# Kernel tuning notes

Measured on AMD Instinct MI355X. Metric: run time of the kernel, lower is better.

Reference implementation:

```python
import jax, jax.numpy as jnp
import numpy as np

B, T, V = 64, 8192, 50257


def setup_inputs() -> dict:
    key = jax.random.key(0)
    k1, k2, k3, k4 = jax.random.split(key, 4)
    ids = jax.random.randint(k1, (B, T), 1, V, dtype=jnp.int32)
    # give each row a random real length in [T//2, T], rest padding (pad_token_id=0)
    lens = jax.random.randint(k4, (B,), T // 2, T + 1, dtype=jnp.int32)
    pos = jnp.arange(T, dtype=jnp.int32)[None, :]
    input_ids = jnp.where(pos < lens[:, None], ids, 0)
    is_punct = jax.random.uniform(k2, (V,)) < 0.05
    is_abbreviation = jax.random.uniform(k3, (V,)) < 0.01
    return {
        "input_ids": input_ids,
        "is_punct": is_punct,
        "is_abbreviation": is_abbreviation,
        "max_phrase_len": 32,
        "pad_token_id": 0,
    }


def reference(input_ids, is_punct, is_abbreviation, max_phrase_len, pad_token_id):
    Bb, Tt = input_ids.shape
    # ---- compute_is_end ----
    punct_at_t = is_punct[input_ids]                               # (B,T)
    prev_ids = jnp.concatenate(
        [jnp.zeros((Bb, 1), input_ids.dtype), input_ids[:, :-1]], axis=1)
    prev_is_abbr = is_abbreviation[prev_ids].at[:, 0].set(False)
    is_real = input_ids != pad_token_id                            # (B,T)
    pos = jnp.arange(Tt, dtype=jnp.int32)
    pos_bt = jnp.broadcast_to(pos[None, :], (Bb, Tt))
    last_real = jnp.max(jnp.where(is_real, pos_bt, -1), axis=1)    # (B,)
    is_end0 = punct_at_t & ~prev_is_abbr & is_real                 # pre-scan boundaries

    def step(last_boundary, xs):
        e_t, t = xs
        forced = (t - last_boundary) >= max_phrase_len
        fire = (e_t | (last_real == t) | forced) & (t <= last_real)
        last_boundary = jnp.where(fire, t, last_boundary)
        return last_boundary, fire

    _, fires = jax.lax.scan(
        step, jnp.full((Bb,), -1, jnp.int32),
        (is_end0.T, jnp.arange(Tt, dtype=jnp.int32)))
    is_end = fires.T                                               # (B,T) bool

    # ---- pack_phrases_from_is_end (P padded to T upper bound) ----
    ie = is_end.astype(jnp.int32)
    phrase_id = jnp.concatenate(
        [jnp.zeros((Bb, 1), jnp.int32), jnp.cumsum(ie[:, :-1], axis=1)], axis=1)
    P = Tt
    rows = jnp.arange(Bb, dtype=jnp.int32)[:, None]
    first_pos = jnp.full((Bb, P), Tt, jnp.int32).at[rows, phrase_id].min(pos_bt)
    slot = pos_bt - jnp.take_along_axis(first_pos, phrase_id, axis=1)  # (B,T)
    in_range = (slot < max_phrase_len) & (slot >= 0) & is_real
    # route invalid entries to a dummy slot (index max_phrase_len), slice it off
    safe_slot = jnp.where(in_range, slot, max_phrase_len)
    mask_pad = jnp.zeros((Bb, P, max_phrase_len + 1), bool)
    mask_pad = mask_pad.at[rows, phrase_id, safe_slot].set(in_range)
    phrase_mask = mask_pad[:, :, :max_phrase_len]
    tok_pad = jnp.zeros((Bb, P, max_phrase_len + 1), jnp.int32)
    tok_pad = tok_pad.at[rows, phrase_id, safe_slot].set(jnp.where(in_range, pos_bt, 0))
    phrase_token_idx = tok_pad[:, :, :max_phrase_len]
    phrase_end_pos = jnp.full((Bb, P), -1, jnp.int32).at[rows, phrase_id].max(
        jnp.where(in_range, pos_bt, -1))
    return phrase_mask, phrase_token_idx, phrase_end_pos
```

## Files before the change

kernel.cpp:

```cpp
#include <hip/hip_runtime.h>
#include <stdint.h>

#define BB 64
#define TT 8192

#define WS_PAIR   4096

#define MOFF ((long long)BB * TT * 32)

__device__ __forceinline__ unsigned long long bitsBelow(int e) {
    return (e >= 64) ? ~0ULL : ((1ULL << e) - 1ULL);
}

__device__ __forceinline__ bool lut(const void* tbl, int flag, int idx) {
    if (flag == 2) return ((const float*)tbl)[idx]   != 0.0f;
    if (flag == 1) return ((const uint8_t*)tbl)[idx] != 0;
    return ((const int*)tbl)[idx] != 0;
}

__global__ __launch_bounds__(256) void bg_kernel(
        const int* __restrict__ ids,
        const void* __restrict__ punct,
        const void* __restrict__ abbr,
        ulonglong2* __restrict__ pairW,
        int* __restrict__ out) {
    __shared__ int sFlag;
    if (threadIdx.x == 0) sFlag = 0;
    __syncthreads();
    {
        const uint32_t* w = (const uint32_t*)punct;
        bool byteGT1 = false, wordGT1 = false;
#pragma unroll
        for (int j = 0; j < 4; ++j) {
            uint32_t x = w[threadIdx.x * 4 + j];
            byteGT1 |= (x & 0xFEFEFEFEu) != 0u;
            wordGT1 |= (x > 1u);
        }
        int local = (byteGT1 ? 2 : 0) | (wordGT1 ? 1 : 0);
        if (local) atomicOr(&sFlag, local);
    }
    __syncthreads();
    int fl = sFlag;
    int flag = (fl & 2) ? 2 : (fl & 1);

    {
        long long zbase = (long long)blockIdx.x * 16384;
        int4 z = make_int4(0, 0, 0, 0);
#pragma unroll
        for (int k = 0; k < 16; ++k) {
            *(int4*)(out + zbase + k * 1024 + threadIdx.x * 4) = z;
        }
        out[2 * MOFF + blockIdx.x * 256 + threadIdx.x] = -1;
    }

    int g = blockIdx.x * 256 + threadIdx.x;
    int t = g & (TT - 1);
    int id = ids[g];
    bool real = (id != 0);
    bool isLR = real && ((t == TT - 1) || (ids[g + 1] == 0));
    bool e = false;
    if (real) {
        bool pu = lut(punct, flag, id);
        if (pu) {
            bool pa = (t > 0) ? lut(abbr, flag, ids[g - 1]) : false;
            e = !pa;
        }
    }
    bool natural = real && (e || isLR);
    unsigned long long nb = __ballot(natural);
    unsigned long long rb = __ballot(real);
    if ((threadIdx.x & 63) == 0) {
        pairW[g >> 6] = make_ulonglong2(nb, rb);
    }
}

__global__ __launch_bounds__(1024) void sparse_kernel(
        const ulonglong2* __restrict__ pairW,
        int* __restrict__ out) {
    __shared__ int sFires[TT];
    __shared__ int sNf;

    int b    = blockIdx.x;
    int tid  = threadIdx.x;
    int wave = tid >> 6, lane = tid & 63;

    if (wave == 0) {
        ulonglong2 pA = pairW[b * 128 + lane];
        ulonglong2 pB = pairW[b * 128 + 64 + lane];
        unsigned long long nA = pA.x, rA = pA.y;
        unsigned long long nB = pB.x, rB = pB.y;
        int lnA = nA ? lane * 64 + 63 - __clzll(nA) : -1;
        int lnB = nB ? (lane + 64) * 64 + 63 - __clzll(nB) : -1;
        int sA = lnA;
        for (int d = 1; d < 64; d <<= 1) { int v = __shfl_up(sA, d); if (lane >= d) sA = max(sA, v); }
        int exA = __shfl_up(sA, 1); if (lane == 0) exA = -1;
        int totA = __shfl(sA, 63);
        int sB = lnB;
        for (int d = 1; d < 64; d <<= 1) { int v = __shfl_up(sB, d); if (lane >= d) sB = max(sB, v); }
        int exB = __shfl_up(sB, 1); if (lane == 0) exB = -1;
        exB = max(exB, totA);

        auto fireWord = [&](unsigned long long nw, unsigned long long rw,
                            int widx, int carry) -> unsigned long long {
            long long wbase = (long long)widx * 64;
            unsigned long long fire = 0, rem = nw;
            long long cur = carry;
            while (true) {
                int nxt = rem ? (__ffsll(rem) - 1) : 64;
                int r = (int)(((cur - wbase) % 32 + 32) % 32);
                unsigned long long pat = (1ULL << r) | (1ULL << (r + 32));
                int s = (int)(cur - wbase + 1); if (s < 0) s = 0;
                fire |= pat & bitsBelow(nxt) & ~bitsBelow(s);
                if (!rem) break;
                fire |= 1ULL << nxt;
                cur = wbase + nxt;
                rem &= rem - 1;
            }
            return fire & rw;
        };
        unsigned long long fA = fireWord(nA, rA, lane, exA);
        unsigned long long fB = fireWord(nB, rB, lane + 64, exB);
        int pcA = __popcll(fA), pcB = __popcll(fB);
        int iA = pcA;
        for (int d = 1; d < 64; d <<= 1) { int v = __shfl_up(iA, d); if (lane >= d) iA += v; }
        int baseA = iA - pcA;
        int totPA = __shfl(iA, 63);
        int iB = pcB;
        for (int d = 1; d < 64; d <<= 1) { int v = __shfl_up(iB, d); if (lane >= d) iB += v; }
        int baseB = totPA + iB - pcB;
        int total = totPA + __shfl(iB, 63);
        unsigned long long f = fA; int idx = baseA;
        while (f) { int t = __ffsll(f) - 1; sFires[idx++] = lane * 64 + t; f &= f - 1; }
        f = fB; idx = baseB;
        while (f) { int t = __ffsll(f) - 1; sFires[idx++] = (lane + 64) * 64 + t; f &= f - 1; }
        if (lane == 0) sNf = total;
    }
    __syncthreads();

    int nf = sNf;
    int ntask = nf * 8;
    for (int task = tid; task < ntask; task += 1024) {
        int q = task & 7;
        int p = task >> 3;
        int end   = sFires[p];
        int start = (p > 0) ? (sFires[p - 1] + 1) : 0;
        int len   = end - start + 1;
        int s0 = q * 4;
        int4 mv, tv;
        int* mp = (int*)&mv;
        int* tp = (int*)&tv;
#pragma unroll
        for (int j = 0; j < 4; ++j) {
            int s = s0 + j;
            bool m = s < len;
            mp[j] = m ? 1 : 0;
            tp[j] = m ? (start + s) : 0;
        }
        long long bp = (long long)b * TT + p;
        *(int4*)(out + bp * 32 + q * 4)        = mv;
        *(int4*)(out + MOFF + bp * 32 + q * 4) = tv;
        if (q == 0) out[2 * MOFF + bp] = end;
    }
}

extern "C" void kernel_launch(void* const* d_in, const int* in_sizes, int n_in,
                              void* d_out, int out_size, void* d_ws, size_t ws_size,
                              hipStream_t stream) {
    const int*  ids   = (const int*)d_in[0];
    const void* punct = d_in[1];
    const void* abbr  = d_in[2];
    char* ws = (char*)d_ws;
    ulonglong2* pairW = (ulonglong2*)(ws + WS_PAIR);
    int* out = (int*)d_out;

    bg_kernel    <<<(BB * TT) / 256, 256, 0, stream>>>(ids, punct, abbr, pairW, out);
    sparse_kernel<<<BB, 1024, 0, stream>>>(pairW, out);
}
```

Before: 31.29 us.

## Fuse bitmap and phrase-packing kernels using a per-row last-block atomic counter

Merges the bitmap-building kernel and the per-row sparse packing kernel into one launch. Each block of 512 threads does its zeroing and ballot work, then bumps a per-row counter; the last of the 16 blocks for a row runs the fire scan and writes that row's phrase entries. This removes the second kernel launch and lets row packing overlap with other blocks' zero-fill. In exchange it adds a memset launch for the counters, relies on acquire/release ordering across blocks, and does the packing stage with half as many threads.

```diff
diff --git a/kernel.cpp b/kernel.cpp
--- a/kernel.cpp
+++ b/kernel.cpp
@@ -4,6 +4,11 @@
 #define BB 64
 #define TT 8192
 
+#define NB   1024
+#define TPB  512
+#define BPR  16
+
+#define WS_CNT    0
 #define WS_PAIR   4096
 
 #define MOFF ((long long)BB * TT * 32)
@@ -18,21 +23,25 @@
     return ((const int*)tbl)[idx] != 0;
 }
 
-__global__ __launch_bounds__(256) void bg_kernel(
+__global__ __launch_bounds__(TPB) void mono_kernel(
         const int* __restrict__ ids,
         const void* __restrict__ punct,
         const void* __restrict__ abbr,
         ulonglong2* __restrict__ pairW,
+        int* __restrict__ rowCnt,
         int* __restrict__ out) {
-    __shared__ int sFlag;
-    if (threadIdx.x == 0) sFlag = 0;
+    __shared__ int sFires[TT];
+    __shared__ int sFlag, sLast, sNf;
+
+    int tid = threadIdx.x;
+    if (tid == 0) sFlag = 0;
     __syncthreads();
     {
         const uint32_t* w = (const uint32_t*)punct;
         bool byteGT1 = false, wordGT1 = false;
 #pragma unroll
-        for (int j = 0; j < 4; ++j) {
-            uint32_t x = w[threadIdx.x * 4 + j];
+        for (int j = 0; j < 2; ++j) {
+            uint32_t x = w[tid * 2 + j];
             byteGT1 |= (x & 0xFEFEFEFEu) != 0u;
             wordGT1 |= (x > 1u);
         }
@@ -44,46 +53,48 @@
     int flag = (fl & 2) ? 2 : (fl & 1);
 
     {
-        long long zbase = (long long)blockIdx.x * 16384;
+        long long zbase = (long long)blockIdx.x * 32768;
         int4 z = make_int4(0, 0, 0, 0);
 #pragma unroll
         for (int k = 0; k < 16; ++k) {
-            *(int4*)(out + zbase + k * 1024 + threadIdx.x * 4) = z;
+            *(int4*)(out + zbase + k * 2048 + tid * 4) = z;
         }
-        out[2 * MOFF + blockIdx.x * 256 + threadIdx.x] = -1;
+        out[2 * MOFF + blockIdx.x * TPB + tid] = -1;
     }
 
-    int g = blockIdx.x * 256 + threadIdx.x;
+    int g = blockIdx.x * TPB + tid;
     int t = g & (TT - 1);
-    int id = ids[g];
-    bool real = (id != 0);
-    bool isLR = real && ((t == TT - 1) || (ids[g + 1] == 0));
-    bool e = false;
-    if (real) {
-        bool pu = lut(punct, flag, id);
-        if (pu) {
-            bool pa = (t > 0) ? lut(abbr, flag, ids[g - 1]) : false;
-            e = !pa;
+    int b = g >> 13;
+    {
+        int id = ids[g];
+        bool real = (id != 0);
+        bool isLR = real && ((t == TT - 1) || (ids[g + 1] == 0));
+        bool e = false;
+        if (real) {
+            bool pu = lut(punct, flag, id);
+            if (pu) {
+                bool pa = (t > 0) ? lut(abbr, flag, ids[g - 1]) : false;
+                e = !pa;
+            }
+        }
+        bool natural = real && (e || isLR);
+        unsigned long long nb = __ballot(natural);
+        unsigned long long rb = __ballot(real);
+        if ((tid & 63) == 0) {
+            pairW[g >> 6] = make_ulonglong2(nb, rb);
         }
     }
-    bool natural = real && (e || isLR);
-    unsigned long long nb = __ballot(natural);
-    unsigned long long rb = __ballot(real);
-    if ((threadIdx.x & 63) == 0) {
-        pairW[g >> 6] = make_ulonglong2(nb, rb);
+    __syncthreads();
+
+    if (tid == 0) {
+        int old = __hip_atomic_fetch_add(&rowCnt[b], 1, __ATOMIC_ACQ_REL,
+                                         __HIP_MEMORY_SCOPE_AGENT);
+        sLast = (old == BPR - 1);
     }
-}
+    __syncthreads();
+    if (!sLast) return;
 
-__global__ __launch_bounds__(1024) void sparse_kernel(
-        const ulonglong2* __restrict__ pairW,
-        int* __restrict__ out) {
-    __shared__ int sFires[TT];
-    __shared__ int sNf;
-
-    int b    = blockIdx.x;
-    int tid  = threadIdx.x;
     int wave = tid >> 6, lane = tid & 63;
-
     if (wave == 0) {
         ulonglong2 pA = pairW[b * 128 + lane];
         ulonglong2 pB = pairW[b * 128 + 64 + lane];
@@ -130,16 +141,16 @@
         int baseB = totPA + iB - pcB;
         int total = totPA + __shfl(iB, 63);
         unsigned long long f = fA; int idx = baseA;
-        while (f) { int t = __ffsll(f) - 1; sFires[idx++] = lane * 64 + t; f &= f - 1; }
+        while (f) { int tt = __ffsll(f) - 1; sFires[idx++] = lane * 64 + tt; f &= f - 1; }
         f = fB; idx = baseB;
-        while (f) { int t = __ffsll(f) - 1; sFires[idx++] = (lane + 64) * 64 + t; f &= f - 1; }
+        while (f) { int tt = __ffsll(f) - 1; sFires[idx++] = (lane + 64) * 64 + tt; f &= f - 1; }
         if (lane == 0) sNf = total;
     }
     __syncthreads();
 
     int nf = sNf;
     int ntask = nf * 8;
-    for (int task = tid; task < ntask; task += 1024) {
+    for (int task = tid; task < ntask; task += TPB) {
         int q = task & 7;
         int p = task >> 3;
         int end   = sFires[p];
@@ -170,9 +181,10 @@
     const void* punct = d_in[1];
     const void* abbr  = d_in[2];
     char* ws = (char*)d_ws;
+    int* rowCnt       = (int*)(ws + WS_CNT);
     ulonglong2* pairW = (ulonglong2*)(ws + WS_PAIR);
     int* out = (int*)d_out;
 
-    bg_kernel    <<<(BB * TT) / 256, 256, 0, stream>>>(ids, punct, abbr, pairW, out);
-    sparse_kernel<<<BB, 1024, 0, stream>>>(pairW, out);
+    hipMemsetAsync(rowCnt, 0, BB * sizeof(int), stream);
+    mono_kernel<<<NB, TPB, 0, stream>>>(ids, punct, abbr, pairW, rowCnt, out);
 }
```

Result: slower. 80.72 us (+158.0%).
